# Kernel tuning notes

Hardware: AMD Instinct MI355X
Metric: run time of the kernel (lower is better)

Reference implementation:

```python
import jax, jax.numpy as jnp
import numpy as np

N = 100000   # input nodes
M = 100000   # output nodes (size = (N, M))
NNZ = 3_200_000  # edges, avg_degree 32
B = 32       # batch
D = 32       # Kaiming channel dim


def setup_inputs() -> dict:
    key = jax.random.key(0)
    k1, k2, k3 = jax.random.split(key, 3)
    # COO indices: row 0 = src (in [0, N)), row 1 = dst (in [0, M))
    indices = jax.random.randint(k1, (2, NNZ), 0, N, dtype=jnp.int32)
    # Kaiming init: randn * sqrt(2/d), as in the torch module when d is given
    values = jax.random.normal(k2, (NNZ,), dtype=jnp.float32) * np.float32((2.0 / D) ** 0.5)
    bias = jnp.zeros((M, 1), dtype=jnp.float32)
    x = jax.random.normal(k3, (B, N, 1), dtype=jnp.float32)
    return {"x": x, "indices": indices, "values": values, "bias": bias}


def reference(x, indices, values, bias):
    # Equivalent of: for each b, sparse.mm(W.T, x[b]) + bias, W in COO (N, M)
    # y[b, m] = sum_{e: dst[e]==m} values[e] * x[b, src[e]] + bias[m]
    src = indices[0]
    dst = indices[1]
    contrib = x[:, src, 0] * values[None, :]           # (B, NNZ) gather-multiply
    y = jax.ops.segment_sum(contrib.T, dst, num_segments=M)  # (M, B) scatter-add
    return (y.T + bias[:, 0][None, :])[..., None]       # (B, M, 1)
```

## Files before the change

kernel.cpp:

```cpp
#include <hip/hip_runtime.h>
#include <hip/hip_fp16.h>
#include <stdint.h>

#define NB 32
#define CSHIFT 8
#define CROWS 256
#define NC_MAX 512
#define NWAVE 16
#define FCHUNK 8192
#define FTHREADS 1024
#define EPT (FCHUNK / FTHREADS)
#define CAP_C 9216
#define EPT2 (CAP_C / FTHREADS)
#define SRC_BITS 18
#define SRC_MASK ((1u << SRC_BITS) - 1)
#define GT 512


__global__ void transpose_x_kernel(const float* __restrict__ x,
                                   __half* __restrict__ xt,
                                   int* __restrict__ zeroRegion, int N) {
    __shared__ float tile[32][33];
    if (blockIdx.x == 0) {
        int i = threadIdx.y * 32 + threadIdx.x;
        for (; i < NC_MAX + 4; i += 256) zeroRegion[i] = 0;
    }
    int n0 = blockIdx.x * 32;
    for (int i = threadIdx.y; i < 32; i += 8) {
        int n = n0 + threadIdx.x;
        tile[i][threadIdx.x] = (n < N) ? x[(size_t)i * N + n] : 0.f;
    }
    __syncthreads();
    for (int i = threadIdx.y; i < 32; i += 8) {
        int n = n0 + i;
        if (n < N) xt[(size_t)n * NB + threadIdx.x] =
            __float2half(tile[threadIdx.x][i]);
    }
}

__global__ __launch_bounds__(1024) void fill_coarse(
        const int* __restrict__ src,
        const int* __restrict__ dst,
        const float* __restrict__ vals,
        int* __restrict__ cCursor,
        uint2* __restrict__ csr,
        int* __restrict__ ovCount,
        int* __restrict__ ovList,
        int nnz) {
    __shared__ uint2 stage[FCHUNK];
    __shared__ unsigned short binOf[FCHUNK];
    __shared__ int lhist[NC_MAX];
    __shared__ int lbase[NC_MAX];
    __shared__ int delta[NC_MAX];
    __shared__ int sscan[NC_MAX];
    int t = threadIdx.x;
    int e0 = blockIdx.x * FCHUNK;
    int chunk = min(FCHUNK, nnz - e0);
    int dcache[EPT], scache[EPT];
    float vcache[EPT];
    for (int i = t; i < NC_MAX; i += FTHREADS) lhist[i] = 0;
    __syncthreads();
#pragma unroll
    for (int q = 0; q < EPT; ++q) {
        int e = e0 + q * FTHREADS + t;
        if (e < nnz) {
            int d = dst[e];
            dcache[q] = d;
            scache[q] = src[e];
            vcache[q] = vals[e];
            atomicAdd(&lhist[d >> CSHIFT], 1);
        } else dcache[q] = -1;
    }
    __syncthreads();
    int v = (t < NC_MAX) ? lhist[t] : 0;
    if (t < NC_MAX) sscan[t] = v;
    __syncthreads();
    for (int off = 1; off < NC_MAX; off <<= 1) {
        int add = (t < NC_MAX && t >= off) ? sscan[t - off] : 0;
        __syncthreads();
        if (t < NC_MAX) sscan[t] += add;
        __syncthreads();
    }
    if (t < NC_MAX) {
        int excl = sscan[t] - v;
        lbase[t] = excl;
        int grel = v ? atomicAdd(&cCursor[t], v) : 0;
        delta[t] = grel - excl;
        lhist[t] = 0;
    }
    __syncthreads();
#pragma unroll
    for (int q = 0; q < EPT; ++q) {
        int d = dcache[q];
        if (d >= 0) {
            int bin = d >> CSHIFT;
            int r = atomicAdd(&lhist[bin], 1);
            int pos = lbase[bin] + r;
            if (delta[bin] + pos < CAP_C) {
                stage[pos] = make_uint2(
                    ((uint32_t)(d & (CROWS - 1)) << SRC_BITS) |
                        (uint32_t)scache[q],
                    __float_as_uint(vcache[q]));
                binOf[pos] = (unsigned short)bin;
            } else {
                binOf[pos] = 0xFFFF;
                int op = atomicAdd(ovCount, 1);
                ovList[op] = e0 + q * FTHREADS + t;
            }
        }
    }
    __syncthreads();
    for (int idx = t; idx < chunk; idx += FTHREADS) {
        unsigned short bo = binOf[idx];
        if (bo != 0xFFFF)
            csr[(size_t)bo * CAP_C + delta[bo] + idx] = stage[idx];
    }
}

__global__ __launch_bounds__(1024) void fill_fine2(
        const int* __restrict__ cCursor,
        const uint2* __restrict__ cCsr,
        uint2* __restrict__ fineCsr,
        int* __restrict__ rowBase,
        int* __restrict__ rowCnt, int M) {
    __shared__ int whist[NWAVE][CROWS];
    __shared__ int fbase[CROWS];
    __shared__ int sscan[CROWS];
    int c = blockIdx.x;
    int n = min(cCursor[c], CAP_C);
    int t = threadIdx.x;
    int w = t >> 6;
    uint2 ec[EPT2];
    for (int i = t; i < NWAVE * CROWS; i += FTHREADS) (&whist[0][0])[i] = 0;
    __syncthreads();
    const uint2* reg = cCsr + (size_t)c * CAP_C;
#pragma unroll
    for (int q = 0; q < EPT2; ++q) {
        int j = q * FTHREADS + t;
        if (j < n) {
            uint2 e = reg[j];
            ec[q] = e;
            atomicAdd(&whist[w][(e.x >> SRC_BITS) & (CROWS - 1)], 1);
        }
    }
    __syncthreads();
    int tot = 0;
    if (t < CROWS) {
#pragma unroll
        for (int w2 = 0; w2 < NWAVE; ++w2) tot += whist[w2][t];
        sscan[t] = tot;
    }
    __syncthreads();
    for (int off = 1; off < CROWS; off <<= 1) {
        int add = (t < CROWS && t >= off) ? sscan[t - off] : 0;
        __syncthreads();
        if (t < CROWS) sscan[t] += add;
        __syncthreads();
    }
    if (t < CROWS) {
        int excl = sscan[t] - tot;
        fbase[t] = excl;
        int m = c * CROWS + t;
        if (m < M) {
            rowBase[m] = c * CAP_C + excl;
            rowCnt[m]  = tot;
        }
        int run = excl;
#pragma unroll
        for (int w2 = 0; w2 < NWAVE; ++w2) {
            int cn = whist[w2][t];
            whist[w2][t] = run;
            run += cn;
        }
    }
    __syncthreads();
#pragma unroll
    for (int q = 0; q < EPT2; ++q) {
        int j = q * FTHREADS + t;
        if (j < n) {
            uint2 e = ec[q];
            int p = atomicAdd(&whist[w][(e.x >> SRC_BITS) & (CROWS - 1)], 1);
            fineCsr[(size_t)c * CAP_C + p] = e;
        }
    }
}

__global__ __launch_bounds__(GT) void row_gather(
        const int* __restrict__ rowBase,
        const int* __restrict__ rowCnt,
        const uint2* __restrict__ csr,
        const __half* __restrict__ xt,
        const float* __restrict__ bias,
        float* __restrict__ out, int M) {
    int g = threadIdx.x >> 5;
    int b = threadIdx.x & 31;
    int m = blockIdx.x * (GT / 32) + g;
    if (m >= M) return;
    int j   = rowBase[m];
    int end = j + rowCnt[m];
    float acc0 = 0.f, acc1 = 0.f;
    for (; j + 8 <= end; j += 8) {
        uint2 e0 = csr[j + 0];
        uint2 e1 = csr[j + 1];
        uint2 e2 = csr[j + 2];
        uint2 e3 = csr[j + 3];
        uint2 e4 = csr[j + 4];
        uint2 e5 = csr[j + 5];
        uint2 e6 = csr[j + 6];
        uint2 e7 = csr[j + 7];
        float x0 = __half2float(xt[(size_t)(e0.x & SRC_MASK) * NB + b]);
        float x1 = __half2float(xt[(size_t)(e1.x & SRC_MASK) * NB + b]);
        float x2 = __half2float(xt[(size_t)(e2.x & SRC_MASK) * NB + b]);
        float x3 = __half2float(xt[(size_t)(e3.x & SRC_MASK) * NB + b]);
        float x4 = __half2float(xt[(size_t)(e4.x & SRC_MASK) * NB + b]);
        float x5 = __half2float(xt[(size_t)(e5.x & SRC_MASK) * NB + b]);
        float x6 = __half2float(xt[(size_t)(e6.x & SRC_MASK) * NB + b]);
        float x7 = __half2float(xt[(size_t)(e7.x & SRC_MASK) * NB + b]);
        acc0 = fmaf(__uint_as_float(e0.y), x0, acc0);
        acc1 = fmaf(__uint_as_float(e1.y), x1, acc1);
        acc0 = fmaf(__uint_as_float(e2.y), x2, acc0);
        acc1 = fmaf(__uint_as_float(e3.y), x3, acc1);
        acc0 = fmaf(__uint_as_float(e4.y), x4, acc0);
        acc1 = fmaf(__uint_as_float(e5.y), x5, acc1);
        acc0 = fmaf(__uint_as_float(e6.y), x6, acc0);
        acc1 = fmaf(__uint_as_float(e7.y), x7, acc1);
    }
    for (; j < end; ++j) {
        uint2 e = csr[j];
        acc0 = fmaf(__uint_as_float(e.y),
                    __half2float(xt[(size_t)(e.x & SRC_MASK) * NB + b]),
                    acc0);
    }
    out[(size_t)b * M + m] = acc0 + acc1 + bias[m];
}

__global__ void fixup_kernel(const int* __restrict__ ovCount,
                             const int* __restrict__ ovList,
                             const int* __restrict__ src,
                             const int* __restrict__ dst,
                             const float* __restrict__ vals,
                             const __half* __restrict__ xt,
                             float* __restrict__ out, int M) {
    long long total = (long long)(*ovCount) * 32;
    long long stride = (long long)gridDim.x * blockDim.x;
    for (long long i = (long long)blockIdx.x * blockDim.x + threadIdx.x;
         i < total; i += stride) {
        int k = (int)(i >> 5);
        int b = (int)(i & 31);
        int e = ovList[k];
        atomicAdd(&out[(size_t)b * M + dst[e]],
                  vals[e] * __half2float(xt[(size_t)src[e] * NB + b]));
    }
}

__global__ void finalize_kernel(const float* __restrict__ yt,
                                const float* __restrict__ bias,
                                float* __restrict__ out, int M) {
    __shared__ float tile[32][33];
    int m0 = blockIdx.x * 32;
    for (int i = threadIdx.y; i < 32; i += 8) {
        int m = m0 + i;
        tile[i][threadIdx.x] = (m < M) ? yt[(size_t)m * NB + threadIdx.x] : 0.f;
    }
    __syncthreads();
    for (int i = threadIdx.y; i < 32; i += 8) {
        int m = m0 + threadIdx.x;
        if (m < M) out[(size_t)i * M + m] = tile[threadIdx.x][i] + bias[m];
    }
}

__global__ void scatter_kernel(const int* __restrict__ src,
                               const int* __restrict__ dst,
                               const float* __restrict__ vals,
                               const __half* __restrict__ xt,
                               float* __restrict__ yt, int nnz) {
    long long tid = (long long)blockIdx.x * blockDim.x + threadIdx.x;
    int e = (int)(tid >> 5);
    if (e >= nnz) return;
    int b = (int)(tid & 31);
    atomicAdd(&yt[(size_t)dst[e] * NB + b],
              vals[e] * __half2float(xt[(size_t)src[e] * NB + b]));
}

extern "C" void kernel_launch(void* const* d_in, const int* in_sizes, int n_in,
                              void* d_out, int out_size, void* d_ws, size_t ws_size,
                              hipStream_t stream) {
    const float* x       = (const float*)d_in[0];
    const int*   indices = (const int*)  d_in[1];
    const float* vals    = (const float*)d_in[2];
    const float* bias    = (const float*)d_in[3];

    float* out = (float*)d_out;

    int nnz = in_sizes[1] / 2;
    int N   = in_sizes[0] / NB;
    int M   = in_sizes[3];

    const int* src = indices;
    const int* dst = indices + nnz;

    int ncoarse = (M + CROWS - 1) >> CSHIFT;

    __half* xt      = (__half*)d_ws;
    int*    cCursor = (int*)(xt + (size_t)N * NB);
    int*    ovCount = cCursor + NC_MAX;
    int*    rowBase = ovCount + 4;
    int*    rowCnt  = rowBase + M;
    int*    ovList  = rowCnt + M;
    uint2*  cCsr    = (uint2*)(((uintptr_t)(ovList + nnz) + 15) &
                               ~(uintptr_t)15);
    uint2*  fineCsr = cCsr + (size_t)ncoarse * CAP_C;

    size_t need = (size_t)((char*)(fineCsr + (size_t)ncoarse * CAP_C) -
                           (char*)d_ws);

    float* yt = (float*)(xt + (size_t)N * NB);
    size_t need_fb = (size_t)((char*)(yt + (size_t)M * NB) - (char*)d_ws);

    if (ws_size >= need && ncoarse <= NC_MAX) {
        transpose_x_kernel<<<(N + 31) / 32, dim3(32, 8), 0, stream>>>(
            x, xt, cCursor, N);
        int fgrid = (nnz + FCHUNK - 1) / FCHUNK;
        fill_coarse<<<fgrid, FTHREADS, 0, stream>>>(src, dst, vals, cCursor,
                                                    cCsr, ovCount, ovList,
                                                    nnz);
        fill_fine2<<<ncoarse, FTHREADS, 0, stream>>>(cCursor, cCsr, fineCsr,
                                                     rowBase, rowCnt, M);
        row_gather<<<(M + GT / 32 - 1) / (GT / 32), GT, 0, stream>>>(
            rowBase, rowCnt, fineCsr, xt, bias, out, M);
        fixup_kernel<<<32, 256, 0, stream>>>(ovCount, ovList, src, dst, vals,
                                             xt, out, M);
    } else if (ws_size >= need_fb) {
        transpose_x_kernel<<<(N + 31) / 32, dim3(32, 8), 0, stream>>>(
            x, xt, cCursor, N);
        hipMemsetAsync(yt, 0, (size_t)M * NB * sizeof(float), stream);
        long long pairs = (long long)nnz * NB;
        int grid = (int)((pairs + 255) / 256);
        scatter_kernel<<<grid, 256, 0, stream>>>(src, dst, vals, xt, yt, nnz);
        finalize_kernel<<<(M + 31) / 32, dim3(32, 8), 0, stream>>>(yt, bias,
                                                                   out, M);
    }
}
```

Measured before the change: 205.1 us.

## Fuse per-region fine sort into gather kernel using LDS-resident sorted edges

Merges the fine-bin sort and the row gather into one kernel. Each block now sorts its coarse region's edges by row inside shared memory, then gathers and writes output rows straight from that LDS copy. This removes the global fineCsr write and re-read, the rowBase/rowCnt arrays and one kernel launch. To fit a region in LDS, coarse regions shrink to 128 rows (capacity 4608, up to 1024 bins), which also simplifies the scan in fill_coarse. The trade-off is fewer, heavier gather blocks with large LDS use, which may lower occupancy for the latency-bound xt gathers.

```diff
diff --git a/kernel.cpp b/kernel.cpp
--- a/kernel.cpp
+++ b/kernel.cpp
@@ -3,18 +3,18 @@
 #include <stdint.h>
 
 #define NB 32
-#define CSHIFT 8
-#define CROWS 256
-#define NC_MAX 512
-#define NWAVE 16
+#define CSHIFT 7
+#define CROWS 128
+#define NC_MAX 1024
 #define FCHUNK 8192
 #define FTHREADS 1024
 #define EPT (FCHUNK / FTHREADS)
-#define CAP_C 9216
-#define EPT2 (CAP_C / FTHREADS)
+#define CAP_C 4608
+#define GTHREADS 512
+#define NGW 8
+#define GEPT ((CAP_C + GTHREADS - 1) / GTHREADS)
 #define SRC_BITS 18
 #define SRC_MASK ((1u << SRC_BITS) - 1)
-#define GT 512
 
 
 __global__ void transpose_x_kernel(const float* __restrict__ x,
@@ -52,13 +52,12 @@
     __shared__ int lhist[NC_MAX];
     __shared__ int lbase[NC_MAX];
     __shared__ int delta[NC_MAX];
-    __shared__ int sscan[NC_MAX];
     int t = threadIdx.x;
     int e0 = blockIdx.x * FCHUNK;
     int chunk = min(FCHUNK, nnz - e0);
     int dcache[EPT], scache[EPT];
     float vcache[EPT];
-    for (int i = t; i < NC_MAX; i += FTHREADS) lhist[i] = 0;
+    lhist[t] = 0;
     __syncthreads();
 #pragma unroll
     for (int q = 0; q < EPT; ++q) {
@@ -72,17 +71,17 @@
         } else dcache[q] = -1;
     }
     __syncthreads();
-    int v = (t < NC_MAX) ? lhist[t] : 0;
-    if (t < NC_MAX) sscan[t] = v;
+    int v = lhist[t];
+    lbase[t] = v;
     __syncthreads();
     for (int off = 1; off < NC_MAX; off <<= 1) {
-        int add = (t < NC_MAX && t >= off) ? sscan[t - off] : 0;
+        int add = (t >= off) ? lbase[t - off] : 0;
         __syncthreads();
-        if (t < NC_MAX) sscan[t] += add;
+        lbase[t] += add;
         __syncthreads();
     }
-    if (t < NC_MAX) {
-        int excl = sscan[t] - v;
+    {
+        int excl = lbase[t] - v;
         lbase[t] = excl;
         int grel = v ? atomicAdd(&cCursor[t], v) : 0;
         delta[t] = grel - excl;
@@ -117,26 +116,27 @@
     }
 }
 
-__global__ __launch_bounds__(1024) void fill_fine2(
+__global__ __launch_bounds__(GTHREADS) void region_sort_gather(
         const int* __restrict__ cCursor,
         const uint2* __restrict__ cCsr,
-        uint2* __restrict__ fineCsr,
-        int* __restrict__ rowBase,
-        int* __restrict__ rowCnt, int M) {
-    __shared__ int whist[NWAVE][CROWS];
-    __shared__ int fbase[CROWS];
-    __shared__ int sscan[CROWS];
+        const __half* __restrict__ xt,
+        const float* __restrict__ bias,
+        float* __restrict__ out, int M) {
+    __shared__ uint2 sorted[CAP_C];
+    __shared__ int whist[NGW][CROWS];
+    __shared__ int rowOff[CROWS];
+    __shared__ int rowCnt[CROWS];
     int c = blockIdx.x;
     int n = min(cCursor[c], CAP_C);
     int t = threadIdx.x;
     int w = t >> 6;
-    uint2 ec[EPT2];
-    for (int i = t; i < NWAVE * CROWS; i += FTHREADS) (&whist[0][0])[i] = 0;
+    uint2 ec[GEPT];
+    for (int i = t; i < NGW * CROWS; i += GTHREADS) (&whist[0][0])[i] = 0;
     __syncthreads();
     const uint2* reg = cCsr + (size_t)c * CAP_C;
 #pragma unroll
-    for (int q = 0; q < EPT2; ++q) {
-        int j = q * FTHREADS + t;
+    for (int q = 0; q < GEPT; ++q) {
+        int j = q * GTHREADS + t;
         if (j < n) {
             uint2 e = reg[j];
             ec[q] = e;
@@ -147,27 +147,23 @@
     int tot = 0;
     if (t < CROWS) {
 #pragma unroll
-        for (int w2 = 0; w2 < NWAVE; ++w2) tot += whist[w2][t];
-        sscan[t] = tot;
+        for (int w2 = 0; w2 < NGW; ++w2) tot += whist[w2][t];
+        rowCnt[t] = tot;
+        rowOff[t] = tot;
     }
     __syncthreads();
     for (int off = 1; off < CROWS; off <<= 1) {
-        int add = (t < CROWS && t >= off) ? sscan[t - off] : 0;
+        int add = (t < CROWS && t >= off) ? rowOff[t - off] : 0;
         __syncthreads();
-        if (t < CROWS) sscan[t] += add;
+        if (t < CROWS) rowOff[t] += add;
         __syncthreads();
     }
     if (t < CROWS) {
-        int excl = sscan[t] - tot;
-        fbase[t] = excl;
-        int m = c * CROWS + t;
-        if (m < M) {
-            rowBase[m] = c * CAP_C + excl;
-            rowCnt[m]  = tot;
-        }
+        int excl = rowOff[t] - rowCnt[t];
+        rowOff[t] = excl;
         int run = excl;
 #pragma unroll
-        for (int w2 = 0; w2 < NWAVE; ++w2) {
+        for (int w2 = 0; w2 < NGW; ++w2) {
             int cn = whist[w2][t];
             whist[w2][t] = run;
             run += cn;
@@ -175,63 +171,57 @@
     }
     __syncthreads();
 #pragma unroll
-    for (int q = 0; q < EPT2; ++q) {
-        int j = q * FTHREADS + t;
+    for (int q = 0; q < GEPT; ++q) {
+        int j = q * GTHREADS + t;
         if (j < n) {
             uint2 e = ec[q];
             int p = atomicAdd(&whist[w][(e.x >> SRC_BITS) & (CROWS - 1)], 1);
-            fineCsr[(size_t)c * CAP_C + p] = e;
-        }
-    }
-}
-
-__global__ __launch_bounds__(GT) void row_gather(
-        const int* __restrict__ rowBase,
-        const int* __restrict__ rowCnt,
-        const uint2* __restrict__ csr,
-        const __half* __restrict__ xt,
-        const float* __restrict__ bias,
-        float* __restrict__ out, int M) {
-    int g = threadIdx.x >> 5;
-    int b = threadIdx.x & 31;
-    int m = blockIdx.x * (GT / 32) + g;
-    if (m >= M) return;
-    int j   = rowBase[m];
-    int end = j + rowCnt[m];
-    float acc0 = 0.f, acc1 = 0.f;
-    for (; j + 8 <= end; j += 8) {
-        uint2 e0 = csr[j + 0];
-        uint2 e1 = csr[j + 1];
-        uint2 e2 = csr[j + 2];
-        uint2 e3 = csr[j + 3];
-        uint2 e4 = csr[j + 4];
-        uint2 e5 = csr[j + 5];
-        uint2 e6 = csr[j + 6];
-        uint2 e7 = csr[j + 7];
-        float x0 = __half2float(xt[(size_t)(e0.x & SRC_MASK) * NB + b]);
-        float x1 = __half2float(xt[(size_t)(e1.x & SRC_MASK) * NB + b]);
-        float x2 = __half2float(xt[(size_t)(e2.x & SRC_MASK) * NB + b]);
-        float x3 = __half2float(xt[(size_t)(e3.x & SRC_MASK) * NB + b]);
-        float x4 = __half2float(xt[(size_t)(e4.x & SRC_MASK) * NB + b]);
-        float x5 = __half2float(xt[(size_t)(e5.x & SRC_MASK) * NB + b]);
-        float x6 = __half2float(xt[(size_t)(e6.x & SRC_MASK) * NB + b]);
-        float x7 = __half2float(xt[(size_t)(e7.x & SRC_MASK) * NB + b]);
-        acc0 = fmaf(__uint_as_float(e0.y), x0, acc0);
-        acc1 = fmaf(__uint_as_float(e1.y), x1, acc1);
-        acc0 = fmaf(__uint_as_float(e2.y), x2, acc0);
-        acc1 = fmaf(__uint_as_float(e3.y), x3, acc1);
-        acc0 = fmaf(__uint_as_float(e4.y), x4, acc0);
-        acc1 = fmaf(__uint_as_float(e5.y), x5, acc1);
-        acc0 = fmaf(__uint_as_float(e6.y), x6, acc0);
-        acc1 = fmaf(__uint_as_float(e7.y), x7, acc1);
-    }
-    for (; j < end; ++j) {
-        uint2 e = csr[j];
-        acc0 = fmaf(__uint_as_float(e.y),
-                    __half2float(xt[(size_t)(e.x & SRC_MASK) * NB + b]),
-                    acc0);
-    }
-    out[(size_t)b * M + m] = acc0 + acc1 + bias[m];
+            sorted[p] = e;
+        }
+    }
+    __syncthreads();
+    int g = t >> 5;
+    int b = t & 31;
+    for (int r = g; r < CROWS; r += GTHREADS / 32) {
+        int m = c * CROWS + r;
+        if (m >= M) break;
+        int jj   = rowOff[r];
+        int jend = jj + rowCnt[r];
+        float acc0 = 0.f, acc1 = 0.f;
+        for (; jj + 8 <= jend; jj += 8) {
+            uint2 e0 = sorted[jj + 0];
+            uint2 e1 = sorted[jj + 1];
+            uint2 e2 = sorted[jj + 2];
+            uint2 e3 = sorted[jj + 3];
+            uint2 e4 = sorted[jj + 4];
+            uint2 e5 = sorted[jj + 5];
+            uint2 e6 = sorted[jj + 6];
+            uint2 e7 = sorted[jj + 7];
+            float x0 = __half2float(xt[(size_t)(e0.x & SRC_MASK) * NB + b]);
+            float x1 = __half2float(xt[(size_t)(e1.x & SRC_MASK) * NB + b]);
+            float x2 = __half2float(xt[(size_t)(e2.x & SRC_MASK) * NB + b]);
+            float x3 = __half2float(xt[(size_t)(e3.x & SRC_MASK) * NB + b]);
+            float x4 = __half2float(xt[(size_t)(e4.x & SRC_MASK) * NB + b]);
+            float x5 = __half2float(xt[(size_t)(e5.x & SRC_MASK) * NB + b]);
+            float x6 = __half2float(xt[(size_t)(e6.x & SRC_MASK) * NB + b]);
+            float x7 = __half2float(xt[(size_t)(e7.x & SRC_MASK) * NB + b]);
+            acc0 = fmaf(__uint_as_float(e0.y), x0, acc0);
+            acc1 = fmaf(__uint_as_float(e1.y), x1, acc1);
+            acc0 = fmaf(__uint_as_float(e2.y), x2, acc0);
+            acc1 = fmaf(__uint_as_float(e3.y), x3, acc1);
+            acc0 = fmaf(__uint_as_float(e4.y), x4, acc0);
+            acc1 = fmaf(__uint_as_float(e5.y), x5, acc1);
+            acc0 = fmaf(__uint_as_float(e6.y), x6, acc0);
+            acc1 = fmaf(__uint_as_float(e7.y), x7, acc1);
+        }
+        for (; jj < jend; ++jj) {
+            uint2 e = sorted[jj];
+            acc0 = fmaf(__uint_as_float(e.y),
+                        __half2float(xt[(size_t)(e.x & SRC_MASK) * NB + b]),
+                        acc0);
+        }
+        out[(size_t)b * M + m] = acc0 + acc1 + bias[m];
+    }
 }
 
 __global__ void fixup_kernel(const int* __restrict__ ovCount,
@@ -304,14 +294,11 @@
     __half* xt      = (__half*)d_ws;
     int*    cCursor = (int*)(xt + (size_t)N * NB);
     int*    ovCount = cCursor + NC_MAX;
-    int*    rowBase = ovCount + 4;
-    int*    rowCnt  = rowBase + M;
-    int*    ovList  = rowCnt + M;
+    int*    ovList  = ovCount + 4;
     uint2*  cCsr    = (uint2*)(((uintptr_t)(ovList + nnz) + 15) &
                                ~(uintptr_t)15);
-    uint2*  fineCsr = cCsr + (size_t)ncoarse * CAP_C;
-
-    size_t need = (size_t)((char*)(fineCsr + (size_t)ncoarse * CAP_C) -
+
+    size_t need = (size_t)((char*)(cCsr + (size_t)ncoarse * CAP_C) -
                            (char*)d_ws);
 
     float* yt = (float*)(xt + (size_t)N * NB);
@@ -324,10 +311,8 @@
         fill_coarse<<<fgrid, FTHREADS, 0, stream>>>(src, dst, vals, cCursor,
                                                     cCsr, ovCount, ovList,
                                                     nnz);
-        fill_fine2<<<ncoarse, FTHREADS, 0, stream>>>(cCursor, cCsr, fineCsr,
-                                                     rowBase, rowCnt, M);
-        row_gather<<<(M + GT / 32 - 1) / (GT / 32), GT, 0, stream>>>(
-            rowBase, rowCnt, fineCsr, xt, bias, out, M);
+        region_sort_gather<<<ncoarse, GTHREADS, 0, stream>>>(cCursor, cCsr,
+                                                             xt, bias, out, M);
         fixup_kernel<<<32, 256, 0, stream>>>(ovCount, ovList, src, dst, vals,
                                              xt, out, M);
     } else if (ws_size >= need_fb) {
```

Result: faster. 194.3 us (-5.3%).
